# Performance work log

Hardware: AMD Instinct MI355X
Metric: run time of the kernel (lower is better)

Reference implementation:

```python
import jax, jax.numpy as jnp
import numpy as np

D = 512
E = 1024
LAMBDA_INIT = 0.05

def setup_inputs() -> dict:
    key = jax.random.key(0)
    ks = jax.random.split(key, 8)
    B, S = 4, 4096
    X = jax.random.normal(ks[0], (B, S, E), dtype=jnp.float32)
    Wq = jax.random.normal(ks[1], (2 * D, E), dtype=jnp.float32) / np.sqrt(E)
    bq = jnp.zeros((2 * D,), dtype=jnp.float32)
    Wk = jax.random.normal(ks[2], (2 * D, E), dtype=jnp.float32) / np.sqrt(E)
    bk = jnp.zeros((2 * D,), dtype=jnp.float32)
    Wv = jax.random.normal(ks[3], (D, E), dtype=jnp.float32) / np.sqrt(E)
    bv = jnp.zeros((D,), dtype=jnp.float32)
    lam = jax.random.normal(ks[4], (1,), dtype=jnp.float32)
    return {"X": X, "Wq": Wq, "bq": bq, "Wk": Wk, "bk": bk, "Wv": Wv, "bv": bv, "lam": lam}

def reference(X, Wq, bq, Wk, bk, Wv, bv, lam):
    # Linear projections (torch Linear: x @ W.T + b)
    Q = jnp.einsum('bse,fe->bsf', X, Wq) + bq   # [B,S,2d]
    K = jnp.einsum('bse,fe->bsf', X, Wk) + bk   # [B,S,2d]
    V = jnp.einsum('bse,de->bsd', X, Wv) + bv   # [B,S,d]
    Q1, Q2 = Q[..., :D], Q[..., D:]
    K1, K2 = K[..., :D], K[..., D:]
    s = 1.0 / np.sqrt(D)
    A1 = jnp.einsum('bqd,bkd->bqk', Q1, K1) * s  # [B,S,S]
    A2 = jnp.einsum('bqd,bkd->bqk', Q2, K2) * s
    P1 = jax.nn.softmax(A1, axis=-1)
    P2 = jax.nn.softmax(A2, axis=-1)
    lambda_ = jnp.exp(lam) + LAMBDA_INIT         # scalar [1]
    diff = P1 - lambda_ * P2
    return jnp.einsum('bqk,bkd->bqd', diff, V)   # [B,S,d]
```

## Files before the change

### kernel.cpp

```cpp
#include <hip/hip_runtime.h>
#include <cstdint>
#include <cstddef>

#define NB    4
#define SEQ   4096
#define EDIM  1024
#define DHEAD 512
#define NTOK  (NB * SEQ)
#define FQK   2048
#define FQKV  2560

typedef __bf16 bf16x8 __attribute__((ext_vector_type(8)));
typedef float  f32x4  __attribute__((ext_vector_type(4)));

__device__ __forceinline__ unsigned short f2bf(float f) {
  union { float f; unsigned int u; } v; v.f = f;
  return (unsigned short)((v.u + 0x7fffu + ((v.u >> 16) & 1u)) >> 16);
}
__device__ __forceinline__ float bf2f(unsigned short h) {
  union { unsigned int u; float f; } v; v.u = ((unsigned int)h) << 16;
  return v.f;
}

__device__ __forceinline__ void gld_lds16(const void* g, void* l) {
  __builtin_amdgcn_global_load_lds(
      (const __attribute__((address_space(1))) unsigned int*)g,
      (__attribute__((address_space(3))) unsigned int*)l, 16, 0, 0);
}

template <class Epi>
__device__ __forceinline__ void gemm_bt_core(
    const unsigned short* __restrict__ A, const unsigned short* __restrict__ B,
    int K, int lda, int ldb, int m0, int n0, Epi epi) {
  __shared__ __align__(16) unsigned short As[2][128 * 32];
  __shared__ __align__(16) unsigned short Bs[2][128 * 32];
  const int t = threadIdx.x;
  const int w = t >> 6;
  const int lane = t & 63;
  const int wr = w >> 1, wc = w & 1;

  f32x4 acc[4][4];
#pragma unroll
  for (int i = 0; i < 4; ++i)
#pragma unroll
    for (int j = 0; j < 4; ++j) acc[i][j] = f32x4{0.f, 0.f, 0.f, 0.f};

  const int c0 = (w * 2) * 64 + lane;
  const int c1 = (w * 2 + 1) * 64 + lane;
  const int r0 = c0 >> 2, col0 = (c0 & 3) * 8;
  const int r1 = c1 >> 2, col1 = (c1 & 3) * 8;
  const int o0 = (w * 2) * 512;
  const int o1 = (w * 2 + 1) * 512;
  const unsigned short* gA0 = A + (size_t)(m0 + r0) * lda + col0;
  const unsigned short* gA1 = A + (size_t)(m0 + r1) * lda + col1;
  const unsigned short* gB0 = B + (size_t)(n0 + r0) * ldb + col0;
  const unsigned short* gB1 = B + (size_t)(n0 + r1) * ldb + col1;

  gld_lds16(gA0, &As[0][o0]);
  gld_lds16(gA1, &As[0][o1]);
  gld_lds16(gB0, &Bs[0][o0]);
  gld_lds16(gB1, &Bs[0][o1]);
  __syncthreads();

  int cur = 0;
  for (int kt = 0; kt < K; kt += 32) {
    const int nxt = cur ^ 1;
    if (kt + 32 < K) {
      gld_lds16(gA0 + kt + 32, &As[nxt][o0]);
      gld_lds16(gA1 + kt + 32, &As[nxt][o1]);
      gld_lds16(gB0 + kt + 32, &Bs[nxt][o0]);
      gld_lds16(gB1 + kt + 32, &Bs[nxt][o1]);
    }
    bf16x8 af[4], bfr[4];
#pragma unroll
    for (int tm = 0; tm < 4; ++tm) {
      int r = wr * 64 + tm * 16 + (lane & 15);
      af[tm] = *(const bf16x8*)&As[cur][r * 32 + (lane >> 4) * 8];
    }
#pragma unroll
    for (int tn = 0; tn < 4; ++tn) {
      int r = wc * 64 + tn * 16 + (lane & 15);
      bfr[tn] = *(const bf16x8*)&Bs[cur][r * 32 + (lane >> 4) * 8];
    }
#pragma unroll
    for (int tm = 0; tm < 4; ++tm)
#pragma unroll
      for (int tn = 0; tn < 4; ++tn)
        acc[tm][tn] = __builtin_amdgcn_mfma_f32_16x16x32_bf16(
            af[tm], bfr[tn], acc[tm][tn], 0, 0, 0);
    __syncthreads();
    cur = nxt;
  }
  epi(acc, wr, wc, lane);
}

__global__ void k_cvt_x(const float* __restrict__ X, unsigned short* __restrict__ Xb) {
  int i = blockIdx.x * blockDim.x + threadIdx.x;
  float4 v = ((const float4*)X)[i];
  ushort4 o;
  o.x = f2bf(v.x); o.y = f2bf(v.y); o.z = f2bf(v.z); o.w = f2bf(v.w);
  ((ushort4*)Xb)[i] = o;
}

__global__ void k_pack_w(const float* __restrict__ Wq, const float* __restrict__ Wk,
                         const float* __restrict__ Wv, unsigned short* __restrict__ Wb) {
  int i = blockIdx.x * blockDim.x + threadIdx.x;
  int idx = i * 4;
  int f = idx >> 10, e = idx & 1023;
  const float* src = (f < 1024) ? (Wq + (size_t)f * 1024)
                   : (f < 2048) ? (Wk + (size_t)(f - 1024) * 1024)
                                : (Wv + (size_t)(f - 2048) * 1024);
  float4 v = *(const float4*)(src + e);
  ushort4 o;
  o.x = f2bf(v.x); o.y = f2bf(v.y); o.z = f2bf(v.z); o.w = f2bf(v.w);
  ((ushort4*)Wb)[i] = o;
}

__global__ void k_pack_b(const float* __restrict__ bq, const float* __restrict__ bk,
                         const float* __restrict__ bv, float* __restrict__ bc) {
  int f = blockIdx.x * blockDim.x + threadIdx.x;
  if (f < FQKV)
    bc[f] = (f < 1024) ? bq[f] : (f < 2048) ? bk[f - 1024] : bv[f - 2048];
}

__global__ void k_zero_f(float* __restrict__ p) {
  int i = blockIdx.x * blockDim.x + threadIdx.x;
  p[i] = 0.f;
}

__global__ __launch_bounds__(256) void k_qk(const unsigned short* __restrict__ Xb,
                                            const unsigned short* __restrict__ Wb,
                                            const float* __restrict__ bc,
                                            unsigned short* __restrict__ QK) {
  const int m0 = blockIdx.y * 128, n0 = blockIdx.x * 128;
  gemm_bt_core(Xb, Wb, EDIM, EDIM, EDIM, m0, n0,
    [&](f32x4 (&acc)[4][4], int wr, int wc, int lane) {
#pragma unroll
      for (int tm = 0; tm < 4; ++tm)
#pragma unroll
        for (int tn = 0; tn < 4; ++tn) {
          int kc = n0 + wc * 64 + tn * 16 + (lane & 15);
          float bias = bc[kc];
#pragma unroll
          for (int i = 0; i < 4; ++i) {
            int q = m0 + wr * 64 + tm * 16 + (lane >> 4) * 4 + i;
            QK[(size_t)q * FQK + kc] = f2bf(acc[tm][tn][i] + bias);
          }
        }
    });
}

__global__ __launch_bounds__(256) void k_v(const unsigned short* __restrict__ Xb,
                                           const unsigned short* __restrict__ Wb,
                                           const float* __restrict__ bc,
                                           unsigned short* __restrict__ Vt) {
  const int b = blockIdx.z;
  const int m0 = blockIdx.y * 128;
  const int n0 = blockIdx.x * 128;
  const unsigned short* A = Wb + (size_t)2048 * EDIM;
  const unsigned short* B = Xb + (size_t)b * SEQ * EDIM;
  unsigned short* Vb = Vt + (size_t)b * DHEAD * SEQ;
  gemm_bt_core(A, B, EDIM, EDIM, EDIM, m0, n0,
    [&](f32x4 (&acc)[4][4], int wr, int wc, int lane) {
#pragma unroll
      for (int tm = 0; tm < 4; ++tm)
#pragma unroll
        for (int tn = 0; tn < 4; ++tn) {
          int s = n0 + wc * 64 + tn * 16 + (lane & 15);
#pragma unroll
          for (int i = 0; i < 4; ++i) {
            int d = m0 + wr * 64 + tm * 16 + (lane >> 4) * 4 + i;
            Vb[(size_t)d * SEQ + s] = f2bf(acc[tm][tn][i] + bc[2048 + d]);
          }
        }
    });
}

__global__ __launch_bounds__(512, 2) void k_scores8(const unsigned short* __restrict__ QK,
                                                    unsigned short* __restrict__ E_c,
                                                    float* __restrict__ ls, int b0) {
  __shared__ __align__(16) unsigned short LA[2][256 * 64];
  __shared__ __align__(16) unsigned short LB[2][256 * 64];
  const int z = blockIdx.z, rb = z >> 1, which = z & 1, b = b0 + rb;
  const int m0 = blockIdx.y * 256, n0 = blockIdx.x * 256;
  const unsigned short* Aq = QK + (size_t)b * SEQ * FQK + which * 512;
  const unsigned short* Bk = Aq + 1024;
  unsigned short* Eb = E_c + (size_t)z * SEQ * SEQ;
  float* lr = ls + (size_t)which * NTOK + (size_t)b * SEQ;
  const int t = threadIdx.x, w = t >> 6, lane = t & 63;
  const int wr = w >> 2, wc = w & 3;
  const int l15 = lane & 15, c16 = lane >> 4, x7 = l15 & 7;

  f32x4 acc[8][4];
#pragma unroll
  for (int i = 0; i < 8; ++i)
#pragma unroll
    for (int j = 0; j < 4; ++j) acc[i][j] = f32x4{0.f, 0.f, 0.f, 0.f};

  unsigned goffA[4], goffB[4]; int loff[4];
#pragma unroll
  for (int i = 0; i < 4; ++i) {
    int c = w * 64 + lane + 512 * i;
    int r = c >> 3;
    int sg = (c & 7) ^ (r & 7);
    goffA[i] = (unsigned)((m0 + r) * FQK + sg * 8);
    goffB[i] = (unsigned)((n0 + r) * FQK + sg * 8);
    loff[i] = (w * 64 + 512 * i) * 8;
  }

  auto STAGE = [&](int buf, int kh) {
#pragma unroll
    for (int i = 0; i < 4; ++i) gld_lds16(Aq + goffA[i] + kh, &LA[buf][loff[i]]);
#pragma unroll
    for (int i = 0; i < 4; ++i) gld_lds16(Bk + goffB[i] + kh, &LB[buf][loff[i]]);
  };

  STAGE(0, 0);
  __syncthreads();

  for (int kt = 0; kt < 8; ++kt) {
    const int cb = kt & 1;
    if (kt < 7) STAGE(cb ^ 1, (kt + 1) * 64);
    __builtin_amdgcn_s_setprio(1);
    bf16x8 bfr[4][2];
#pragma unroll
    for (int tn = 0; tn < 4; ++tn)
#pragma unroll
      for (int ks = 0; ks < 2; ++ks)
        bfr[tn][ks] = *(const bf16x8*)
            &LB[cb][(wc * 64 + tn * 16 + l15) * 64 + (((ks * 4 + c16) ^ x7) * 8)];
#pragma unroll
    for (int mh = 0; mh < 2; ++mh) {
      bf16x8 af[4][2];
#pragma unroll
      for (int tq = 0; tq < 4; ++tq)
#pragma unroll
        for (int ks = 0; ks < 2; ++ks)
          af[tq][ks] = *(const bf16x8*)
              &LA[cb][(wr * 128 + mh * 64 + tq * 16 + l15) * 64 + (((ks * 4 + c16) ^ x7) * 8)];
#pragma unroll
      for (int tq = 0; tq < 4; ++tq)
#pragma unroll
        for (int tn = 0; tn < 4; ++tn)
#pragma unroll
          for (int ks = 0; ks < 2; ++ks)
            acc[mh * 4 + tq][tn] = __builtin_amdgcn_mfma_f32_16x16x32_bf16(
                af[tq][ks], bfr[tn][ks], acc[mh * 4 + tq][tn], 0, 0, 0);
    }
    __builtin_amdgcn_s_setprio(0);
    __syncthreads();
  }

  const float scale = 0.04419417382415922f;
  float rs[8][4];
#pragma unroll
  for (int tm = 0; tm < 8; ++tm)
#pragma unroll
    for (int i = 0; i < 4; ++i) rs[tm][i] = 0.f;
#pragma unroll
  for (int tm = 0; tm < 8; ++tm)
#pragma unroll
    for (int tn = 0; tn < 4; ++tn) {
      int k = n0 + wc * 64 + tn * 16 + l15;
#pragma unroll
      for (int i = 0; i < 4; ++i) {
        int q = m0 + wr * 128 + tm * 16 + c16 * 4 + i;
        float e = __expf(acc[tm][tn][i] * scale);
        unsigned short eb = f2bf(e);
        Eb[(size_t)q * SEQ + k] = eb;
        rs[tm][i] += bf2f(eb);
      }
    }
#pragma unroll
  for (int tm = 0; tm < 8; ++tm)
#pragma unroll
    for (int i = 0; i < 4; ++i) {
      float v = rs[tm][i];
      v += __shfl_xor(v, 1);
      v += __shfl_xor(v, 2);
      v += __shfl_xor(v, 4);
      v += __shfl_xor(v, 8);
      rs[tm][i] = v;
    }
  if (l15 == 0) {
#pragma unroll
    for (int tm = 0; tm < 8; ++tm)
#pragma unroll
      for (int i = 0; i < 4; ++i) {
        int q = m0 + wr * 128 + tm * 16 + c16 * 4 + i;
        atomicAdd(&lr[q], rs[tm][i]);
      }
  }
}

__global__ __launch_bounds__(512, 2) void k_pv8(const unsigned short* __restrict__ E_c,
                                                const unsigned short* __restrict__ Vt,
                                                float* __restrict__ O12, int b0) {
  __shared__ __align__(16) unsigned short LA[2][256 * 64];
  __shared__ __align__(16) unsigned short LB[2][128 * 64];
  const int z = blockIdx.z, b = b0 + (z >> 1);
  const int q0 = blockIdx.y * 256, n0 = blockIdx.x * 128;
  const unsigned short* Ae = E_c + (size_t)z * SEQ * SEQ;
  const unsigned short* Bv = Vt + (size_t)b * DHEAD * SEQ;
  float* Ob = O12 + (size_t)z * SEQ * DHEAD;
  const int t = threadIdx.x, w = t >> 6, lane = t & 63;
  const int wr = w >> 1, wc = w & 1;
  const int l15 = lane & 15, c16 = lane >> 4, x7 = l15 & 7;

  f32x4 acc[4][4];
#pragma unroll
  for (int i = 0; i < 4; ++i)
#pragma unroll
    for (int j = 0; j < 4; ++j) acc[i][j] = f32x4{0.f, 0.f, 0.f, 0.f};

  unsigned goffE[4], goffV[2]; int loffE[4], loffV[2];
#pragma unroll
  for (int i = 0; i < 4; ++i) {
    int c = w * 64 + lane + 512 * i;
    int r = c >> 3;
    int sg = (c & 7) ^ (r & 7);
    goffE[i] = (unsigned)((q0 + r) * SEQ + sg * 8);
    loffE[i] = (w * 64 + 512 * i) * 8;
  }
#pragma unroll
  for (int i = 0; i < 2; ++i) {
    int c = w * 64 + lane + 512 * i;
    int r = c >> 3;
    int sg = (c & 7) ^ (r & 7);
    goffV[i] = (unsigned)((n0 + r) * SEQ + sg * 8);
    loffV[i] = (w * 64 + 512 * i) * 8;
  }

  auto STAGE = [&](int buf, int kh) {
#pragma unroll
    for (int i = 0; i < 4; ++i) gld_lds16(Ae + goffE[i] + kh, &LA[buf][loffE[i]]);
#pragma unroll
    for (int i = 0; i < 2; ++i) gld_lds16(Bv + goffV[i] + kh, &LB[buf][loffV[i]]);
  };

  STAGE(0, 0);
  __syncthreads();

  for (int kt = 0; kt < 64; ++kt) {
    const int cb = kt & 1;
    if (kt < 63) STAGE(cb ^ 1, (kt + 1) * 64);
    __builtin_amdgcn_s_setprio(1);
    bf16x8 af[4][2], bfr[4][2];
#pragma unroll
    for (int tn = 0; tn < 4; ++tn)
#pragma unroll
      for (int ks = 0; ks < 2; ++ks)
        bfr[tn][ks] = *(const bf16x8*)
            &LB[cb][(wc * 64 + tn * 16 + l15) * 64 + (((ks * 4 + c16) ^ x7) * 8)];
#pragma unroll
    for (int tq = 0; tq < 4; ++tq)
#pragma unroll
      for (int ks = 0; ks < 2; ++ks)
        af[tq][ks] = *(const bf16x8*)
            &LA[cb][(wr * 64 + tq * 16 + l15) * 64 + (((ks * 4 + c16) ^ x7) * 8)];
#pragma unroll
    for (int tq = 0; tq < 4; ++tq)
#pragma unroll
      for (int tn = 0; tn < 4; ++tn)
#pragma unroll
        for (int ks = 0; ks < 2; ++ks)
          acc[tq][tn] = __builtin_amdgcn_mfma_f32_16x16x32_bf16(
              af[tq][ks], bfr[tn][ks], acc[tq][tn], 0, 0, 0);
    __builtin_amdgcn_s_setprio(0);
    __syncthreads();
  }

#pragma unroll
  for (int tq = 0; tq < 4; ++tq)
#pragma unroll
    for (int tn = 0; tn < 4; ++tn) {
      int d = n0 + wc * 64 + tn * 16 + l15;
#pragma unroll
      for (int i = 0; i < 4; ++i) {
        int q = q0 + wr * 64 + tq * 16 + c16 * 4 + i;
        Ob[(size_t)q * DHEAD + d] = acc[tq][tn][i];
      }
    }
}

__global__ void k_combine(const float* __restrict__ O12, const float* __restrict__ ls,
                          const float* __restrict__ lam, float* __restrict__ out, int b0) {
  int i = blockIdx.x * blockDim.x + threadIdx.x;
  float lambda = expf(lam[0]) + 0.05f;
  int gq = i >> 7;
  int rb = gq >> 12;
  int q = gq & 4095;
  int dv = i & 127;
  int b = b0 + rb;
  float inv1 = 1.f / ls[(size_t)b * SEQ + q];
  float inv2 = lambda / ls[NTOK + (size_t)b * SEQ + q];
  size_t ai = (size_t)(rb * 2) * (SEQ * 128) + (size_t)q * 128 + dv;
  float4 a = ((const float4*)O12)[ai];
  float4 c = ((const float4*)O12)[ai + SEQ * 128];
  float4 r;
  r.x = a.x * inv1 - c.x * inv2;
  r.y = a.y * inv1 - c.y * inv2;
  r.z = a.z * inv1 - c.z * inv2;
  r.w = a.w * inv1 - c.w * inv2;
  ((float4*)out)[(size_t)(b * SEQ + q) * 128 + dv] = r;
}

extern "C" void kernel_launch(void* const* d_in, const int* in_sizes, int n_in,
                              void* d_out, int out_size, void* d_ws, size_t ws_size,
                              hipStream_t stream) {
  const float* X   = (const float*)d_in[0];
  const float* Wq  = (const float*)d_in[1];
  const float* bq  = (const float*)d_in[2];
  const float* Wk  = (const float*)d_in[3];
  const float* bk  = (const float*)d_in[4];
  const float* Wv  = (const float*)d_in[5];
  const float* bv  = (const float*)d_in[6];
  const float* lam = (const float*)d_in[7];
  float* out = (float*)d_out;

  char* ws = (char*)d_ws;
  size_t off = 0;
  auto alloc = [&](size_t b) { size_t r = off; off += (b + 255) & ~(size_t)255; return r; };
  unsigned short* Xb  = (unsigned short*)(ws + alloc((size_t)NTOK * EDIM * 2));
  unsigned short* Wb  = (unsigned short*)(ws + alloc((size_t)FQKV * EDIM * 2));
  float*          bc  = (float*)(ws + alloc((size_t)FQKV * 4));
  unsigned short* QK  = (unsigned short*)(ws + alloc((size_t)NTOK * FQK * 2));
  unsigned short* Vt  = (unsigned short*)(ws + alloc((size_t)NB * DHEAD * SEQ * 2));
  unsigned short* E_c = (unsigned short*)(ws + alloc((size_t)4 * SEQ * SEQ * 2));
  float*          ls  = (float*)(ws + alloc((size_t)2 * NTOK * 4));
  float* O12 = (float*)Xb;

  k_cvt_x<<<dim3((NTOK * EDIM / 4) / 256), dim3(256), 0, stream>>>(X, Xb);
  k_pack_w<<<dim3((FQKV * EDIM / 4) / 256), dim3(256), 0, stream>>>(Wq, Wk, Wv, Wb);
  k_pack_b<<<dim3(10), dim3(256), 0, stream>>>(bq, bk, bv, bc);
  k_qk<<<dim3(FQK / 128, NTOK / 128), dim3(256), 0, stream>>>(Xb, Wb, bc, QK);
  k_v<<<dim3(SEQ / 128, DHEAD / 128, NB), dim3(256), 0, stream>>>(Xb, Wb, bc, Vt);
  k_zero_f<<<dim3(2 * NTOK / 256), dim3(256), 0, stream>>>(ls);
  for (int b0 = 0; b0 < NB; b0 += 2) {
    k_scores8<<<dim3(SEQ / 256, SEQ / 256, 4), dim3(512), 0, stream>>>(QK, E_c, ls, b0);
    k_pv8<<<dim3(DHEAD / 128, SEQ / 256, 4), dim3(512), 0, stream>>>(E_c, Vt, O12, b0);
    k_combine<<<dim3((2 * SEQ * DHEAD / 4) / 256), dim3(256), 0, stream>>>(O12, ls, lam, out, b0);
  }

  (void)in_sizes; (void)n_in; (void)out_size; (void)ws_size;
}
```

Measured before the change: 689.3 us.

## Shrink attention GEMM tiles, swizzle LDS in projection GEMM, raise occupancy

```diff
diff --git a/kernel.cpp b/kernel.cpp
--- a/kernel.cpp
+++ b/kernel.cpp
@@ -16,10 +16,6 @@
 __device__ __forceinline__ unsigned short f2bf(float f) {
   union { float f; unsigned int u; } v; v.f = f;
   return (unsigned short)((v.u + 0x7fffu + ((v.u >> 16) & 1u)) >> 16);
-}
-__device__ __forceinline__ float bf2f(unsigned short h) {
-  union { unsigned int u; float f; } v; v.u = ((unsigned int)h) << 16;
-  return v.f;
 }
 
 __device__ __forceinline__ void gld_lds16(const void* g, void* l) {
@@ -38,6 +34,7 @@
   const int w = t >> 6;
   const int lane = t & 63;
   const int wr = w >> 1, wc = w & 1;
+  const int l15 = lane & 15, c16 = lane >> 4, x3 = l15 & 3;
 
   f32x4 acc[4][4];
 #pragma unroll
@@ -45,16 +42,16 @@
 #pragma unroll
     for (int j = 0; j < 4; ++j) acc[i][j] = f32x4{0.f, 0.f, 0.f, 0.f};
 
-  const int c0 = (w * 2) * 64 + lane;
-  const int c1 = (w * 2 + 1) * 64 + lane;
-  const int r0 = c0 >> 2, col0 = (c0 & 3) * 8;
-  const int r1 = c1 >> 2, col1 = (c1 & 3) * 8;
-  const int o0 = (w * 2) * 512;
-  const int o1 = (w * 2 + 1) * 512;
-  const unsigned short* gA0 = A + (size_t)(m0 + r0) * lda + col0;
-  const unsigned short* gA1 = A + (size_t)(m0 + r1) * lda + col1;
-  const unsigned short* gB0 = B + (size_t)(n0 + r0) * ldb + col0;
-  const unsigned short* gB1 = B + (size_t)(n0 + r1) * ldb + col1;
+  const int c0 = w * 128 + lane;
+  const int c1 = w * 128 + 64 + lane;
+  const int r0 = c0 >> 2, s0 = (c0 & 3) ^ (r0 & 3);
+  const int r1 = c1 >> 2, s1 = (c1 & 3) ^ (r1 & 3);
+  const int o0 = (w * 128) * 8;
+  const int o1 = (w * 128 + 64) * 8;
+  const unsigned short* gA0 = A + (size_t)(m0 + r0) * lda + s0 * 8;
+  const unsigned short* gA1 = A + (size_t)(m0 + r1) * lda + s1 * 8;
+  const unsigned short* gB0 = B + (size_t)(n0 + r0) * ldb + s0 * 8;
+  const unsigned short* gB1 = B + (size_t)(n0 + r1) * ldb + s1 * 8;
 
   gld_lds16(gA0, &As[0][o0]);
   gld_lds16(gA1, &As[0][o1]);
@@ -71,16 +68,17 @@
       gld_lds16(gB0 + kt + 32, &Bs[nxt][o0]);
       gld_lds16(gB1 + kt + 32, &Bs[nxt][o1]);
     }
+    __builtin_amdgcn_s_setprio(1);
     bf16x8 af[4], bfr[4];
 #pragma unroll
     for (int tm = 0; tm < 4; ++tm) {
-      int r = wr * 64 + tm * 16 + (lane & 15);
-      af[tm] = *(const bf16x8*)&As[cur][r * 32 + (lane >> 4) * 8];
+      int r = wr * 64 + tm * 16 + l15;
+      af[tm] = *(const bf16x8*)&As[cur][r * 32 + ((c16 ^ x3) * 8)];
     }
 #pragma unroll
     for (int tn = 0; tn < 4; ++tn) {
-      int r = wc * 64 + tn * 16 + (lane & 15);
-      bfr[tn] = *(const bf16x8*)&Bs[cur][r * 32 + (lane >> 4) * 8];
+      int r = wc * 64 + tn * 16 + l15;
+      bfr[tn] = *(const bf16x8*)&Bs[cur][r * 32 + ((c16 ^ x3) * 8)];
     }
 #pragma unroll
     for (int tm = 0; tm < 4; ++tm)
@@ -88,6 +86,7 @@
       for (int tn = 0; tn < 4; ++tn)
         acc[tm][tn] = __builtin_amdgcn_mfma_f32_16x16x32_bf16(
             af[tm], bfr[tn], acc[tm][tn], 0, 0, 0);
+    __builtin_amdgcn_s_setprio(0);
     __syncthreads();
     cur = nxt;
   }
@@ -144,7 +143,8 @@
 #pragma unroll
           for (int i = 0; i < 4; ++i) {
             int q = m0 + wr * 64 + tm * 16 + (lane >> 4) * 4 + i;
-            QK[(size_t)q * FQK + kc] = f2bf(acc[tm][tn][i] + bias);
+            __bf16 h = (__bf16)(acc[tm][tn][i] + bias);
+            QK[(size_t)q * FQK + kc] = *(const unsigned short*)&h;
           }
         }
     });
@@ -170,109 +170,104 @@
 #pragma unroll
           for (int i = 0; i < 4; ++i) {
             int d = m0 + wr * 64 + tm * 16 + (lane >> 4) * 4 + i;
-            Vb[(size_t)d * SEQ + s] = f2bf(acc[tm][tn][i] + bc[2048 + d]);
+            __bf16 h = (__bf16)(acc[tm][tn][i] + bc[2048 + d]);
+            Vb[(size_t)d * SEQ + s] = *(const unsigned short*)&h;
           }
         }
     });
 }
 
-__global__ __launch_bounds__(512, 2) void k_scores8(const unsigned short* __restrict__ QK,
+__global__ __launch_bounds__(512, 6) void k_scores9(const unsigned short* __restrict__ QK,
                                                     unsigned short* __restrict__ E_c,
                                                     float* __restrict__ ls, int b0) {
-  __shared__ __align__(16) unsigned short LA[2][256 * 64];
-  __shared__ __align__(16) unsigned short LB[2][256 * 64];
+  __shared__ __align__(16) unsigned short LA[2][256 * 32];
+  __shared__ __align__(16) unsigned short LB[2][128 * 32];
   const int z = blockIdx.z, rb = z >> 1, which = z & 1, b = b0 + rb;
-  const int m0 = blockIdx.y * 256, n0 = blockIdx.x * 256;
+  const int m0 = blockIdx.y * 256, n0 = blockIdx.x * 128;
   const unsigned short* Aq = QK + (size_t)b * SEQ * FQK + which * 512;
   const unsigned short* Bk = Aq + 1024;
   unsigned short* Eb = E_c + (size_t)z * SEQ * SEQ;
   float* lr = ls + (size_t)which * NTOK + (size_t)b * SEQ;
   const int t = threadIdx.x, w = t >> 6, lane = t & 63;
-  const int wr = w >> 2, wc = w & 3;
-  const int l15 = lane & 15, c16 = lane >> 4, x7 = l15 & 7;
-
-  f32x4 acc[8][4];
-#pragma unroll
-  for (int i = 0; i < 8; ++i)
+  const int wr = w >> 1, wc = w & 1;
+  const int l15 = lane & 15, c16 = lane >> 4, x3 = l15 & 3;
+
+  f32x4 acc[4][4];
+#pragma unroll
+  for (int i = 0; i < 4; ++i)
 #pragma unroll
     for (int j = 0; j < 4; ++j) acc[i][j] = f32x4{0.f, 0.f, 0.f, 0.f};
 
-  unsigned goffA[4], goffB[4]; int loff[4];
-#pragma unroll
-  for (int i = 0; i < 4; ++i) {
-    int c = w * 64 + lane + 512 * i;
-    int r = c >> 3;
-    int sg = (c & 7) ^ (r & 7);
+  unsigned goffA[2]; int loffA[2];
+#pragma unroll
+  for (int i = 0; i < 2; ++i) {
+    int c = w * 128 + 64 * i + lane;
+    int r = c >> 2;
+    int sg = (c & 3) ^ (r & 3);
     goffA[i] = (unsigned)((m0 + r) * FQK + sg * 8);
-    goffB[i] = (unsigned)((n0 + r) * FQK + sg * 8);
-    loff[i] = (w * 64 + 512 * i) * 8;
-  }
-
-  auto STAGE = [&](int buf, int kh) {
-#pragma unroll
-    for (int i = 0; i < 4; ++i) gld_lds16(Aq + goffA[i] + kh, &LA[buf][loff[i]]);
-#pragma unroll
-    for (int i = 0; i < 4; ++i) gld_lds16(Bk + goffB[i] + kh, &LB[buf][loff[i]]);
+    loffA[i] = (w * 128 + 64 * i) * 8;
+  }
+  const int cB = w * 64 + lane;
+  const int rB = cB >> 2, sB = (cB & 3) ^ (rB & 3);
+  const unsigned goffB = (unsigned)((n0 + rB) * FQK + sB * 8);
+  const int loffB = (w * 64) * 8;
+
+  auto STAGE = [&](int buf, int kt) {
+#pragma unroll
+    for (int i = 0; i < 2; ++i) gld_lds16(Aq + goffA[i] + kt * 32, &LA[buf][loffA[i]]);
+    gld_lds16(Bk + goffB + kt * 32, &LB[buf][loffB]);
   };
 
   STAGE(0, 0);
   __syncthreads();
 
-  for (int kt = 0; kt < 8; ++kt) {
+  for (int kt = 0; kt < 16; ++kt) {
     const int cb = kt & 1;
-    if (kt < 7) STAGE(cb ^ 1, (kt + 1) * 64);
+    if (kt < 15) STAGE(cb ^ 1, kt + 1);
     __builtin_amdgcn_s_setprio(1);
-    bf16x8 bfr[4][2];
-#pragma unroll
-    for (int tn = 0; tn < 4; ++tn)
-#pragma unroll
-      for (int ks = 0; ks < 2; ++ks)
-        bfr[tn][ks] = *(const bf16x8*)
-            &LB[cb][(wc * 64 + tn * 16 + l15) * 64 + (((ks * 4 + c16) ^ x7) * 8)];
-#pragma unroll
-    for (int mh = 0; mh < 2; ++mh) {
-      bf16x8 af[4][2];
-#pragma unroll
-      for (int tq = 0; tq < 4; ++tq)
-#pragma unroll
-        for (int ks = 0; ks < 2; ++ks)
-          af[tq][ks] = *(const bf16x8*)
-              &LA[cb][(wr * 128 + mh * 64 + tq * 16 + l15) * 64 + (((ks * 4 + c16) ^ x7) * 8)];
-#pragma unroll
-      for (int tq = 0; tq < 4; ++tq)
-#pragma unroll
-        for (int tn = 0; tn < 4; ++tn)
-#pragma unroll
-          for (int ks = 0; ks < 2; ++ks)
-            acc[mh * 4 + tq][tn] = __builtin_amdgcn_mfma_f32_16x16x32_bf16(
-                af[tq][ks], bfr[tn][ks], acc[mh * 4 + tq][tn], 0, 0, 0);
-    }
+    bf16x8 af[4], bfr[4];
+#pragma unroll
+    for (int tm = 0; tm < 4; ++tm) {
+      int r = wr * 64 + tm * 16 + l15;
+      af[tm] = *(const bf16x8*)&LA[cb][r * 32 + ((c16 ^ x3) * 8)];
+    }
+#pragma unroll
+    for (int tn = 0; tn < 4; ++tn) {
+      int r = wc * 64 + tn * 16 + l15;
+      bfr[tn] = *(const bf16x8*)&LB[cb][r * 32 + ((c16 ^ x3) * 8)];
+    }
+#pragma unroll
+    for (int tm = 0; tm < 4; ++tm)
+#pragma unroll
+      for (int tn = 0; tn < 4; ++tn)
+        acc[tm][tn] = __builtin_amdgcn_mfma_f32_16x16x32_bf16(
+            af[tm], bfr[tn], acc[tm][tn], 0, 0, 0);
     __builtin_amdgcn_s_setprio(0);
     __syncthreads();
   }
 
   const float scale = 0.04419417382415922f;
-  float rs[8][4];
-#pragma unroll
-  for (int tm = 0; tm < 8; ++tm)
+  float rs[4][4];
+#pragma unroll
+  for (int tm = 0; tm < 4; ++tm)
 #pragma unroll
     for (int i = 0; i < 4; ++i) rs[tm][i] = 0.f;
 #pragma unroll
-  for (int tm = 0; tm < 8; ++tm)
+  for (int tm = 0; tm < 4; ++tm)
 #pragma unroll
     for (int tn = 0; tn < 4; ++tn) {
       int k = n0 + wc * 64 + tn * 16 + l15;
 #pragma unroll
       for (int i = 0; i < 4; ++i) {
-        int q = m0 + wr * 128 + tm * 16 + c16 * 4 + i;
+        int q = m0 + wr * 64 + tm * 16 + c16 * 4 + i;
         float e = __expf(acc[tm][tn][i] * scale);
-        unsigned short eb = f2bf(e);
-        Eb[(size_t)q * SEQ + k] = eb;
-        rs[tm][i] += bf2f(eb);
+        __bf16 h = (__bf16)e;
+        Eb[(size_t)q * SEQ + k] = *(const unsigned short*)&h;
+        rs[tm][i] += (float)h;
       }
     }
 #pragma unroll
-  for (int tm = 0; tm < 8; ++tm)
+  for (int tm = 0; tm < 4; ++tm)
 #pragma unroll
     for (int i = 0; i < 4; ++i) {
       float v = rs[tm][i];
@@ -284,28 +279,28 @@
     }
   if (l15 == 0) {
 #pragma unroll
-    for (int tm = 0; tm < 8; ++tm)
+    for (int tm = 0; tm < 4; ++tm)
 #pragma unroll
       for (int i = 0; i < 4; ++i) {
-        int q = m0 + wr * 128 + tm * 16 + c16 * 4 + i;
+        int q = m0 + wr * 64 + tm * 16 + c16 * 4 + i;
         atomicAdd(&lr[q], rs[tm][i]);
       }
   }
 }
 
-__global__ __launch_bounds__(512, 2) void k_pv8(const unsigned short* __restrict__ E_c,
+__global__ __launch_bounds__(256, 5) void k_pv9(const unsigned short* __restrict__ E_c,
                                                 const unsigned short* __restrict__ Vt,
                                                 float* __restrict__ O12, int b0) {
-  __shared__ __align__(16) unsigned short LA[2][256 * 64];
-  __shared__ __align__(16) unsigned short LB[2][128 * 64];
+  __shared__ __align__(16) unsigned short LA[2][128 * 32];
+  __shared__ __align__(16) unsigned short LB[2][128 * 32];
   const int z = blockIdx.z, b = b0 + (z >> 1);
-  const int q0 = blockIdx.y * 256, n0 = blockIdx.x * 128;
+  const int q0 = blockIdx.y * 128, n0 = blockIdx.x * 128;
   const unsigned short* Ae = E_c + (size_t)z * SEQ * SEQ;
   const unsigned short* Bv = Vt + (size_t)b * DHEAD * SEQ;
   float* Ob = O12 + (size_t)z * SEQ * DHEAD;
   const int t = threadIdx.x, w = t >> 6, lane = t & 63;
   const int wr = w >> 1, wc = w & 1;
-  const int l15 = lane & 15, c16 = lane >> 4, x7 = l15 & 7;
+  const int l15 = lane & 15, c16 = lane >> 4, x3 = l15 & 3;
 
   f32x4 acc[4][4];
 #pragma unroll
@@ -313,59 +308,49 @@
 #pragma unroll
     for (int j = 0; j < 4; ++j) acc[i][j] = f32x4{0.f, 0.f, 0.f, 0.f};
 
-  unsigned goffE[4], goffV[2]; int loffE[4], loffV[2];
-#pragma unroll
-  for (int i = 0; i < 4; ++i) {
-    int c = w * 64 + lane + 512 * i;
-    int r = c >> 3;
-    int sg = (c & 7) ^ (r & 7);
+  unsigned goffE[2], goffV[2]; int loff[2];
+#pragma unroll
+  for (int i = 0; i < 2; ++i) {
+    int c = w * 128 + 64 * i + lane;
+    int r = c >> 2;
+    int sg = (c & 3) ^ (r & 3);
     goffE[i] = (unsigned)((q0 + r) * SEQ + sg * 8);
-    loffE[i] = (w * 64 + 512 * i) * 8;
-  }
-#pragma unroll
-  for (int i = 0; i < 2; ++i) {
-    int c = w * 64 + lane + 512 * i;
-    int r = c >> 3;
-    int sg = (c & 7) ^ (r & 7);
     goffV[i] = (unsigned)((n0 + r) * SEQ + sg * 8);
-    loffV[i] = (w * 64 + 512 * i) * 8;
-  }
-
-  auto STAGE = [&](int buf, int kh) {
-#pragma unroll
-    for (int i = 0; i < 4; ++i) gld_lds16(Ae + goffE[i] + kh, &LA[buf][loffE[i]]);
-#pragma unroll
-    for (int i = 0; i < 2; ++i) gld_lds16(Bv + goffV[i] + kh, &LB[buf][loffV[i]]);
+    loff[i] = (w * 128 + 64 * i) * 8;
+  }
+
+  auto STAGE = [&](int buf, int kt) {
+#pragma unroll
+    for (int i = 0; i < 2; ++i) {
+      gld_lds16(Ae + goffE[i] + kt * 32, &LA[buf][loff[i]]);
+      gld_lds16(Bv + goffV[i] + kt * 32, &LB[buf][loff[i]]);
+    }
   };
 
   STAGE(0, 0);
   __syncthreads();
 
-  for (int kt = 0; kt < 64; ++kt) {
+  for (int kt = 0; kt < 128; ++kt) {
     const int cb = kt & 1;
-    if (kt < 63) STAGE(cb ^ 1, (kt + 1) * 64);
+    if (kt < 127) STAGE(cb ^ 1, kt + 1);
     __builtin_amdgcn_s_setprio(1);
-    bf16x8 af[4][2], bfr[4][2];
-#pragma unroll
-    for (int tn = 0; tn < 4; ++tn)
-#pragma unroll
-      for (int ks = 0; ks < 2; ++ks)
-        bfr[tn][ks] = *(const bf16x8*)
-            &LB[cb][(wc * 64 + tn * 16 + l15) * 64 + (((ks * 4 + c16) ^ x7) * 8)];
+    bf16x8 af[4], bfr[4];
+#pragma unroll
+    for (int tq = 0; tq < 4; ++tq) {
+      int r = wr * 64 + tq * 16 + l15;
+      af[tq] = *(const bf16x8*)&LA[cb][r * 32 + ((c16 ^ x3) * 8)];
+    }
+#pragma unroll
+    for (int tn = 0; tn < 4; ++tn) {
+      int r = wc * 64 + tn * 16 + l15;
+      bfr[tn] = *(const bf16x8*)&LB[cb][r * 32 + ((c16 ^ x3) * 8)];
+    }
 #pragma unroll
     for (int tq = 0; tq < 4; ++tq)
 #pragma unroll
-      for (int ks = 0; ks < 2; ++ks)
-        af[tq][ks] = *(const bf16x8*)
-            &LA[cb][(wr * 64 + tq * 16 + l15) * 64 + (((ks * 4 + c16) ^ x7) * 8)];
-#pragma unroll
-    for (int tq = 0; tq < 4; ++tq)
-#pragma unroll
       for (int tn = 0; tn < 4; ++tn)
-#pragma unroll
-        for (int ks = 0; ks < 2; ++ks)
-          acc[tq][tn] = __builtin_amdgcn_mfma_f32_16x16x32_bf16(
-              af[tq][ks], bfr[tn][ks], acc[tq][tn], 0, 0, 0);
+        acc[tq][tn] = __builtin_amdgcn_mfma_f32_16x16x32_bf16(
+            af[tq], bfr[tn], acc[tq][tn], 0, 0, 0);
     __builtin_amdgcn_s_setprio(0);
     __syncthreads();
   }
@@ -437,8 +422,8 @@
   k_v<<<dim3(SEQ / 128, DHEAD / 128, NB), dim3(256), 0, stream>>>(Xb, Wb, bc, Vt);
   k_zero_f<<<dim3(2 * NTOK / 256), dim3(256), 0, stream>>>(ls);
   for (int b0 = 0; b0 < NB; b0 += 2) {
-    k_scores8<<<dim3(SEQ / 256, SEQ / 256, 4), dim3(512), 0, stream>>>(QK, E_c, ls, b0);
-    k_pv8<<<dim3(DHEAD / 128, SEQ / 256, 4), dim3(512), 0, stream>>>(E_c, Vt, O12, b0);
+    k_scores9<<<dim3(SEQ / 128, SEQ / 256, 4), dim3(512), 0, stream>>>(QK, E_c, ls, b0);
+    k_pv9<<<dim3(DHEAD / 128, SEQ / 128, 4), dim3(256), 0, stream>>>(E_c, Vt, O12, b0);
     k_combine<<<dim3((2 * SEQ * DHEAD / 4) / 256), dim3(256), 0, stream>>>(O12, ls, lam, out, b0);
   }
 
```

Result: slower. 1.467 ms (+112.9%).

## Use partial vmcnt waits, swizzle projection GEMM LDS, and hardware bf16 converts

Applied to the files above, without the earlier changes.

```diff
diff --git a/kernel.cpp b/kernel.cpp
--- a/kernel.cpp
+++ b/kernel.cpp
@@ -13,13 +13,12 @@
 typedef __bf16 bf16x8 __attribute__((ext_vector_type(8)));
 typedef float  f32x4  __attribute__((ext_vector_type(4)));
 
+#define WAITCNT(VM) asm volatile("s_waitcnt vmcnt(" #VM ") lgkmcnt(0)" ::: "memory")
+#define BAR() __builtin_amdgcn_s_barrier()
+
 __device__ __forceinline__ unsigned short f2bf(float f) {
   union { float f; unsigned int u; } v; v.f = f;
   return (unsigned short)((v.u + 0x7fffu + ((v.u >> 16) & 1u)) >> 16);
-}
-__device__ __forceinline__ float bf2f(unsigned short h) {
-  union { unsigned int u; float f; } v; v.u = ((unsigned int)h) << 16;
-  return v.f;
 }
 
 __device__ __forceinline__ void gld_lds16(const void* g, void* l) {
@@ -38,6 +37,7 @@
   const int w = t >> 6;
   const int lane = t & 63;
   const int wr = w >> 1, wc = w & 1;
+  const int l15 = lane & 15, c16 = lane >> 4, x3 = l15 & 3;
 
   f32x4 acc[4][4];
 #pragma unroll
@@ -45,42 +45,42 @@
 #pragma unroll
     for (int j = 0; j < 4; ++j) acc[i][j] = f32x4{0.f, 0.f, 0.f, 0.f};
 
-  const int c0 = (w * 2) * 64 + lane;
-  const int c1 = (w * 2 + 1) * 64 + lane;
-  const int r0 = c0 >> 2, col0 = (c0 & 3) * 8;
-  const int r1 = c1 >> 2, col1 = (c1 & 3) * 8;
-  const int o0 = (w * 2) * 512;
-  const int o1 = (w * 2 + 1) * 512;
-  const unsigned short* gA0 = A + (size_t)(m0 + r0) * lda + col0;
-  const unsigned short* gA1 = A + (size_t)(m0 + r1) * lda + col1;
-  const unsigned short* gB0 = B + (size_t)(n0 + r0) * ldb + col0;
-  const unsigned short* gB1 = B + (size_t)(n0 + r1) * ldb + col1;
-
-  gld_lds16(gA0, &As[0][o0]);
-  gld_lds16(gA1, &As[0][o1]);
-  gld_lds16(gB0, &Bs[0][o0]);
-  gld_lds16(gB1, &Bs[0][o1]);
-  __syncthreads();
-
-  int cur = 0;
-  for (int kt = 0; kt < K; kt += 32) {
-    const int nxt = cur ^ 1;
-    if (kt + 32 < K) {
-      gld_lds16(gA0 + kt + 32, &As[nxt][o0]);
-      gld_lds16(gA1 + kt + 32, &As[nxt][o1]);
-      gld_lds16(gB0 + kt + 32, &Bs[nxt][o0]);
-      gld_lds16(gB1 + kt + 32, &Bs[nxt][o1]);
-    }
+  const int c0 = w * 128 + lane;
+  const int c1 = w * 128 + 64 + lane;
+  const int r0 = c0 >> 2, s0 = (c0 & 3) ^ (r0 & 3);
+  const int r1 = c1 >> 2, s1 = (c1 & 3) ^ (r1 & 3);
+  const int o0 = (w * 128) * 8;
+  const int o1 = (w * 128 + 64) * 8;
+  const unsigned short* gA0 = A + (size_t)(m0 + r0) * lda + s0 * 8;
+  const unsigned short* gA1 = A + (size_t)(m0 + r1) * lda + s1 * 8;
+  const unsigned short* gB0 = B + (size_t)(n0 + r0) * ldb + s0 * 8;
+  const unsigned short* gB1 = B + (size_t)(n0 + r1) * ldb + s1 * 8;
+
+  auto STAGE = [&](int buf, int kt) {
+    gld_lds16(gA0 + kt, &As[buf][o0]);
+    gld_lds16(gA1 + kt, &As[buf][o1]);
+    gld_lds16(gB0 + kt, &Bs[buf][o0]);
+    gld_lds16(gB1 + kt, &Bs[buf][o1]);
+  };
+
+  STAGE(0, 0);
+  const int NT = K >> 5;
+  for (int tt = 0; tt < NT; ++tt) {
+    const int cb = tt & 1;
+    if (tt + 1 < NT) { STAGE(cb ^ 1, (tt + 1) * 32); WAITCNT(4); }
+    else             { WAITCNT(0); }
+    BAR();
+    __builtin_amdgcn_s_setprio(1);
     bf16x8 af[4], bfr[4];
 #pragma unroll
     for (int tm = 0; tm < 4; ++tm) {
-      int r = wr * 64 + tm * 16 + (lane & 15);
-      af[tm] = *(const bf16x8*)&As[cur][r * 32 + (lane >> 4) * 8];
+      int r = wr * 64 + tm * 16 + l15;
+      af[tm] = *(const bf16x8*)&As[cb][r * 32 + ((c16 ^ x3) * 8)];
     }
 #pragma unroll
     for (int tn = 0; tn < 4; ++tn) {
-      int r = wc * 64 + tn * 16 + (lane & 15);
-      bfr[tn] = *(const bf16x8*)&Bs[cur][r * 32 + (lane >> 4) * 8];
+      int r = wc * 64 + tn * 16 + l15;
+      bfr[tn] = *(const bf16x8*)&Bs[cb][r * 32 + ((c16 ^ x3) * 8)];
     }
 #pragma unroll
     for (int tm = 0; tm < 4; ++tm)
@@ -88,8 +88,8 @@
       for (int tn = 0; tn < 4; ++tn)
         acc[tm][tn] = __builtin_amdgcn_mfma_f32_16x16x32_bf16(
             af[tm], bfr[tn], acc[tm][tn], 0, 0, 0);
-    __syncthreads();
-    cur = nxt;
+    __builtin_amdgcn_s_setprio(0);
+    BAR();
   }
   epi(acc, wr, wc, lane);
 }
@@ -144,7 +144,8 @@
 #pragma unroll
           for (int i = 0; i < 4; ++i) {
             int q = m0 + wr * 64 + tm * 16 + (lane >> 4) * 4 + i;
-            QK[(size_t)q * FQK + kc] = f2bf(acc[tm][tn][i] + bias);
+            __bf16 h = (__bf16)(acc[tm][tn][i] + bias);
+            QK[(size_t)q * FQK + kc] = *(const unsigned short*)&h;
           }
         }
     });
@@ -170,7 +171,8 @@
 #pragma unroll
           for (int i = 0; i < 4; ++i) {
             int d = m0 + wr * 64 + tm * 16 + (lane >> 4) * 4 + i;
-            Vb[(size_t)d * SEQ + s] = f2bf(acc[tm][tn][i] + bc[2048 + d]);
+            __bf16 h = (__bf16)(acc[tm][tn][i] + bc[2048 + d]);
+            Vb[(size_t)d * SEQ + s] = *(const unsigned short*)&h;
           }
         }
     });
@@ -216,11 +218,11 @@
   };
 
   STAGE(0, 0);
-  __syncthreads();
-
   for (int kt = 0; kt < 8; ++kt) {
     const int cb = kt & 1;
-    if (kt < 7) STAGE(cb ^ 1, (kt + 1) * 64);
+    if (kt < 7) { STAGE(cb ^ 1, (kt + 1) * 64); WAITCNT(8); }
+    else        { WAITCNT(0); }
+    BAR();
     __builtin_amdgcn_s_setprio(1);
     bf16x8 bfr[4][2];
 #pragma unroll
@@ -248,7 +250,7 @@
                 af[tq][ks], bfr[tn][ks], acc[mh * 4 + tq][tn], 0, 0, 0);
     }
     __builtin_amdgcn_s_setprio(0);
-    __syncthreads();
+    BAR();
   }
 
   const float scale = 0.04419417382415922f;
@@ -266,9 +268,9 @@
       for (int i = 0; i < 4; ++i) {
         int q = m0 + wr * 128 + tm * 16 + c16 * 4 + i;
         float e = __expf(acc[tm][tn][i] * scale);
-        unsigned short eb = f2bf(e);
-        Eb[(size_t)q * SEQ + k] = eb;
-        rs[tm][i] += bf2f(eb);
+        __bf16 h = (__bf16)e;
+        Eb[(size_t)q * SEQ + k] = *(const unsigned short*)&h;
+        rs[tm][i] += (float)h;
       }
     }
 #pragma unroll
@@ -339,11 +341,11 @@
   };
 
   STAGE(0, 0);
-  __syncthreads();
-
   for (int kt = 0; kt < 64; ++kt) {
     const int cb = kt & 1;
-    if (kt < 63) STAGE(cb ^ 1, (kt + 1) * 64);
+    if (kt < 63) { STAGE(cb ^ 1, (kt + 1) * 64); WAITCNT(6); }
+    else         { WAITCNT(0); }
+    BAR();
     __builtin_amdgcn_s_setprio(1);
     bf16x8 af[4][2], bfr[4][2];
 #pragma unroll
@@ -367,7 +369,7 @@
           acc[tq][tn] = __builtin_amdgcn_mfma_f32_16x16x32_bf16(
               af[tq][ks], bfr[tn][ks], acc[tq][tn], 0, 0, 0);
     __builtin_amdgcn_s_setprio(0);
-    __syncthreads();
+    BAR();
   }
 
 #pragma unroll
```

After: 689.8 us. No clear change (+0.1%).
